# Kernel tuning notes

Measured on AMD Instinct MI355X. Metric: run time of the kernel, lower is better.

The kernel has to match this reference:

```python
import jax, jax.numpy as jnp
import numpy as np

B = 8192          # batch size
D = 128           # embedding_dim
R = 1000          # relation_dict_len
MARGIN = 1.0


def setup_inputs() -> dict:
    key = jax.random.key(0)
    k1, k2, k3, k4 = jax.random.split(key, 4)
    return {
        "positive_batch": jax.random.normal(k1, (B, 3, D), dtype=jnp.float32),
        "negative_batch": jax.random.normal(k2, (B, 3, D), dtype=jnp.float32),
        "r_idx": jax.random.randint(k3, (B,), 0, R),
        "rel_emb": jax.random.normal(k4, (R, D * D), dtype=jnp.float32),
    }


def _score(batch, Wr):
    # batch: (B, 3, D) -> h, r, t each (B, D); Wr: (B, D, D)
    h, r, t = batch[:, 0], batch[:, 1], batch[:, 2]
    d = jnp.abs(h + r - t)                       # (B, D)
    # x^T Wr x quadratic form per example, fused in one einsum
    return jnp.einsum('bi,bij,bj->b', d, Wr, d)  # (B,)


def reference(positive_batch, negative_batch, r_idx, rel_emb):
    # Gather per-example relation matrix (Wr built from positive relation,
    # reused for the negative score, as in the original module).
    Wr = rel_emb[r_idx].reshape(-1, D, D)        # (B, D, D)
    pos = _score(positive_batch, Wr)
    neg = _score(negative_batch, Wr)
    return jnp.mean(jax.nn.relu(MARGIN + pos - neg))
```

## Files before the change

kernel.cpp:

```cpp
#include <hip/hip_runtime.h>

#define BATCH 8192
#define DIM 128
#define NREL 1000
#define MARGIN 1.0f

#define WS_PA 0
#define WS_PB 8192
#define WS_ORDER 16384
#define ORDER_CAP 11264

__global__ __launch_bounds__(1024) void sort_kernel(const int* __restrict__ r_idx,
                                                    int* __restrict__ order) {
  __shared__ int s_cnt[1024];
  __shared__ int s_cur[1024];
  __shared__ int s_wsum[16];
  const int tid = threadIdx.x, lane = tid & 63, wave = tid >> 6;
  s_cnt[tid] = 0;
  __syncthreads();
  int my[8];
#pragma unroll
  for (int k = 0; k < 8; ++k) {
    my[k] = r_idx[tid + k * 1024];
    atomicAdd(&s_cnt[my[k]], 1);
  }
  __syncthreads();
  const int c = (s_cnt[tid] + 3) & ~3;
  int v = c;
#pragma unroll
  for (int o = 1; o < 64; o <<= 1) {
    int u = __shfl_up(v, o, 64);
    if (lane >= o) v += u;
  }
  if (lane == 63) s_wsum[wave] = v;
  __syncthreads();
  int woff = 0;
  for (int w = 0; w < wave; ++w) woff += s_wsum[w];
  s_cur[tid] = woff + v - c;
  for (int i = tid; i < ORDER_CAP; i += 1024) order[i] = -1;
  __syncthreads();
#pragma unroll
  for (int k = 0; k < 8; ++k) {
    int p = atomicAdd(&s_cur[my[k]], 1);
    order[p] = tid + k * 1024;
  }
}

__device__ inline float2 dvec(const float* __restrict__ b, int c0) {
  float2 h = *(const float2*)(b + c0);
  float2 r = *(const float2*)(b + DIM + c0);
  float2 t = *(const float2*)(b + 2 * DIM + c0);
  return make_float2(fabsf(h.x + r.x - t.x), fabsf(h.y + r.y - t.y));
}

__global__ __launch_bounds__(256) void score_kernel(
    const float* __restrict__ pos_b, const float* __restrict__ neg_b,
    const int* __restrict__ r_idx, const float* __restrict__ rel_emb,
    const int* __restrict__ order, float* __restrict__ pA,
    float* __restrict__ pB) {
  __shared__ float s_d[4][DIM][8];
  const int tid = threadIdx.x, lane = tid & 63, wave = tid >> 6;
  const int pair = wave >> 1, half = wave & 1;
  const int g = blockIdx.x * 2 + pair;
  int4 es = *(const int4*)(order + g * 4);
  if (es.x < 0) return;
  const int c0 = lane * 2;
  const int r = r_idx[es.x];
  const bool v1 = es.y >= 0, v2 = es.z >= 0, v3 = es.w >= 0;
  const int e1 = v1 ? es.y : es.x, e2 = v2 ? es.z : es.x, e3 = v3 ? es.w : es.x;

  const float2 z = make_float2(0.f, 0.f);
  float2 dp0 = dvec(pos_b + (size_t)es.x * 3 * DIM, c0);
  float2 dn0 = dvec(neg_b + (size_t)es.x * 3 * DIM, c0);
  float2 dp1 = v1 ? dvec(pos_b + (size_t)e1 * 3 * DIM, c0) : z;
  float2 dn1 = v1 ? dvec(neg_b + (size_t)e1 * 3 * DIM, c0) : z;
  float2 dp2 = v2 ? dvec(pos_b + (size_t)e2 * 3 * DIM, c0) : z;
  float2 dn2 = v2 ? dvec(neg_b + (size_t)e2 * 3 * DIM, c0) : z;
  float2 dp3 = v3 ? dvec(pos_b + (size_t)e3 * 3 * DIM, c0) : z;
  float2 dn3 = v3 ? dvec(neg_b + (size_t)e3 * 3 * DIM, c0) : z;

  *(float4*)&s_d[wave][c0][0]     = make_float4(dp0.x, dp1.x, dp2.x, dp3.x);
  *(float4*)&s_d[wave][c0][4]     = make_float4(dn0.x, dn1.x, dn2.x, dn3.x);
  *(float4*)&s_d[wave][c0 + 1][0] = make_float4(dp0.y, dp1.y, dp2.y, dp3.y);
  *(float4*)&s_d[wave][c0 + 1][4] = make_float4(dn0.y, dn1.y, dn2.y, dn3.y);

  const int colb = (lane & 31) * 4;
  const int rsel = lane >> 5;
  const int rowbase = half * 64;
  const float* W = rel_emb + (size_t)r * (DIM * DIM) +
                   (size_t)(rowbase + rsel) * DIM + colb;

  float4 fz = make_float4(0.f, 0.f, 0.f, 0.f);
  float4 ap0 = fz, ap1 = fz, ap2 = fz, ap3 = fz;
  float4 an0 = fz, an1 = fz, an2 = fz, an3 = fz;
#pragma unroll 4
  for (int it = 0; it < 32; ++it) {
    float4 wv = *(const float4*)(W + (size_t)(it * 2) * DIM);
    const int row = rowbase + it * 2 + rsel;
    float4 ddp = *(const float4*)&s_d[wave][row][0];
    float4 ddn = *(const float4*)&s_d[wave][row][4];
    ap0.x = fmaf(ddp.x, wv.x, ap0.x); ap0.y = fmaf(ddp.x, wv.y, ap0.y);
    ap0.z = fmaf(ddp.x, wv.z, ap0.z); ap0.w = fmaf(ddp.x, wv.w, ap0.w);
    ap1.x = fmaf(ddp.y, wv.x, ap1.x); ap1.y = fmaf(ddp.y, wv.y, ap1.y);
    ap1.z = fmaf(ddp.y, wv.z, ap1.z); ap1.w = fmaf(ddp.y, wv.w, ap1.w);
    ap2.x = fmaf(ddp.z, wv.x, ap2.x); ap2.y = fmaf(ddp.z, wv.y, ap2.y);
    ap2.z = fmaf(ddp.z, wv.z, ap2.z); ap2.w = fmaf(ddp.z, wv.w, ap2.w);
    ap3.x = fmaf(ddp.w, wv.x, ap3.x); ap3.y = fmaf(ddp.w, wv.y, ap3.y);
    ap3.z = fmaf(ddp.w, wv.z, ap3.z); ap3.w = fmaf(ddp.w, wv.w, ap3.w);
    an0.x = fmaf(ddn.x, wv.x, an0.x); an0.y = fmaf(ddn.x, wv.y, an0.y);
    an0.z = fmaf(ddn.x, wv.z, an0.z); an0.w = fmaf(ddn.x, wv.w, an0.w);
    an1.x = fmaf(ddn.y, wv.x, an1.x); an1.y = fmaf(ddn.y, wv.y, an1.y);
    an1.z = fmaf(ddn.y, wv.z, an1.z); an1.w = fmaf(ddn.y, wv.w, an1.w);
    an2.x = fmaf(ddn.z, wv.x, an2.x); an2.y = fmaf(ddn.z, wv.y, an2.y);
    an2.z = fmaf(ddn.z, wv.z, an2.z); an2.w = fmaf(ddn.z, wv.w, an2.w);
    an3.x = fmaf(ddn.w, wv.x, an3.x); an3.y = fmaf(ddn.w, wv.y, an3.y);
    an3.z = fmaf(ddn.w, wv.z, an3.z); an3.w = fmaf(ddn.w, wv.w, an3.w);
  }

  float s0 = 0.f, s1 = 0.f, s2 = 0.f, s3 = 0.f;
#define EPI(K, COMP)                                          \
  {                                                           \
    float4 dp4 = *(const float4*)&s_d[wave][colb + K][0];     \
    float4 dn4 = *(const float4*)&s_d[wave][colb + K][4];     \
    s0 += ap0.COMP * dp4.x - an0.COMP * dn4.x;                \
    s1 += ap1.COMP * dp4.y - an1.COMP * dn4.y;                \
    s2 += ap2.COMP * dp4.z - an2.COMP * dn4.z;                \
    s3 += ap3.COMP * dp4.w - an3.COMP * dn4.w;                \
  }
  EPI(0, x) EPI(1, y) EPI(2, z) EPI(3, w)
#undef EPI

#pragma unroll
  for (int o = 32; o > 0; o >>= 1) {
    s0 += __shfl_xor(s0, o, 64);
    s1 += __shfl_xor(s1, o, 64);
    s2 += __shfl_xor(s2, o, 64);
    s3 += __shfl_xor(s3, o, 64);
  }
  float* P = half ? pB : pA;
  if (lane == 0) {
    P[es.x] = s0;
    if (v1) P[es.y] = s1;
    if (v2) P[es.z] = s2;
    if (v3) P[es.w] = s3;
  }
}

__global__ __launch_bounds__(256) void reduce_kernel(const float* __restrict__ pA,
                                                     const float* __restrict__ pB,
                                                     float* __restrict__ out) {
  float acc = 0.f;
  for (int i = threadIdx.x; i < BATCH; i += 256) {
    float v = MARGIN + pA[i] + pB[i];
    acc += (v > 0.f) ? v : 0.f;
  }
#pragma unroll
  for (int o = 32; o > 0; o >>= 1) acc += __shfl_xor(acc, o, 64);
  __shared__ float s[4];
  const int lane = threadIdx.x & 63, wave = threadIdx.x >> 6;
  if (lane == 0) s[wave] = acc;
  __syncthreads();
  if (threadIdx.x == 0) out[0] = (s[0] + s[1] + s[2] + s[3]) * (1.0f / BATCH);
}

extern "C" void kernel_launch(void* const* d_in, const int* in_sizes, int n_in,
                              void* d_out, int out_size, void* d_ws, size_t ws_size,
                              hipStream_t stream) {
  const float* pos_b = (const float*)d_in[0];
  const float* neg_b = (const float*)d_in[1];
  const int* r_idx = (const int*)d_in[2];
  const float* rel_emb = (const float*)d_in[3];
  float* out = (float*)d_out;

  float* pA = (float*)d_ws + WS_PA;
  float* pB = (float*)d_ws + WS_PB;
  int* order = (int*)d_ws + WS_ORDER;

  sort_kernel<<<1, 1024, 0, stream>>>(r_idx, order);
  score_kernel<<<1400, 256, 0, stream>>>(pos_b, neg_b, r_idx, rel_emb, order,
                                         pA, pB);
  reduce_kernel<<<1, 256, 0, stream>>>(pA, pB, out);
}
```

Measured before the change: 46.45 us.

## Fuse final reduction into score kernel via last-block counter and remap blocks

Removes the separate reduce kernel launch by having the last score block, detected through an atomic counter reset in the sort kernel, perform the final ReLU-mean reduction. It also permutes the block-to-work mapping so consecutive physical blocks are spread across the sorted relation groups, presumably to balance load across XCDs. This adds an atomic plus fences per block and a serialized tail reduction on one block, in exchange for saving a launch gap.

```diff
diff --git a/kernel.cpp b/kernel.cpp
--- a/kernel.cpp
+++ b/kernel.cpp
@@ -4,18 +4,22 @@
 #define DIM 128
 #define NREL 1000
 #define MARGIN 1.0f
+#define GRID 1400
 
 #define WS_PA 0
 #define WS_PB 8192
 #define WS_ORDER 16384
+#define WS_CTR 27648
 #define ORDER_CAP 11264
 
 __global__ __launch_bounds__(1024) void sort_kernel(const int* __restrict__ r_idx,
-                                                    int* __restrict__ order) {
+                                                    int* __restrict__ order,
+                                                    int* __restrict__ ctr) {
   __shared__ int s_cnt[1024];
   __shared__ int s_cur[1024];
   __shared__ int s_wsum[16];
   const int tid = threadIdx.x, lane = tid & 63, wave = tid >> 6;
+  if (tid == 0) ctr[0] = 0;
   s_cnt[tid] = 0;
   __syncthreads();
   int my[8];
@@ -57,110 +61,121 @@
     const float* __restrict__ pos_b, const float* __restrict__ neg_b,
     const int* __restrict__ r_idx, const float* __restrict__ rel_emb,
     const int* __restrict__ order, float* __restrict__ pA,
-    float* __restrict__ pB) {
+    float* __restrict__ pB, int* __restrict__ ctr, float* __restrict__ out) {
   __shared__ float s_d[4][DIM][8];
+  __shared__ int s_last;
   const int tid = threadIdx.x, lane = tid & 63, wave = tid >> 6;
+  const int phys = blockIdx.x;
+  const int lb = (phys & 7) * (GRID / 8) + (phys >> 3);
   const int pair = wave >> 1, half = wave & 1;
-  const int g = blockIdx.x * 2 + pair;
+  const int g = lb * 2 + pair;
   int4 es = *(const int4*)(order + g * 4);
-  if (es.x < 0) return;
-  const int c0 = lane * 2;
-  const int r = r_idx[es.x];
-  const bool v1 = es.y >= 0, v2 = es.z >= 0, v3 = es.w >= 0;
-  const int e1 = v1 ? es.y : es.x, e2 = v2 ? es.z : es.x, e3 = v3 ? es.w : es.x;
 
-  const float2 z = make_float2(0.f, 0.f);
-  float2 dp0 = dvec(pos_b + (size_t)es.x * 3 * DIM, c0);
-  float2 dn0 = dvec(neg_b + (size_t)es.x * 3 * DIM, c0);
-  float2 dp1 = v1 ? dvec(pos_b + (size_t)e1 * 3 * DIM, c0) : z;
-  float2 dn1 = v1 ? dvec(neg_b + (size_t)e1 * 3 * DIM, c0) : z;
-  float2 dp2 = v2 ? dvec(pos_b + (size_t)e2 * 3 * DIM, c0) : z;
-  float2 dn2 = v2 ? dvec(neg_b + (size_t)e2 * 3 * DIM, c0) : z;
-  float2 dp3 = v3 ? dvec(pos_b + (size_t)e3 * 3 * DIM, c0) : z;
-  float2 dn3 = v3 ? dvec(neg_b + (size_t)e3 * 3 * DIM, c0) : z;
+  if (es.x >= 0) {
+    const int c0 = lane * 2;
+    const int r = r_idx[es.x];
+    const bool v1 = es.y >= 0, v2 = es.z >= 0, v3 = es.w >= 0;
+    const int e1 = v1 ? es.y : es.x, e2 = v2 ? es.z : es.x,
+              e3 = v3 ? es.w : es.x;
 
-  *(float4*)&s_d[wave][c0][0]     = make_float4(dp0.x, dp1.x, dp2.x, dp3.x);
-  *(float4*)&s_d[wave][c0][4]     = make_float4(dn0.x, dn1.x, dn2.x, dn3.x);
-  *(float4*)&s_d[wave][c0 + 1][0] = make_float4(dp0.y, dp1.y, dp2.y, dp3.y);
-  *(float4*)&s_d[wave][c0 + 1][4] = make_float4(dn0.y, dn1.y, dn2.y, dn3.y);
+    const float2 z = make_float2(0.f, 0.f);
+    float2 dp0 = dvec(pos_b + (size_t)es.x * 3 * DIM, c0);
+    float2 dn0 = dvec(neg_b + (size_t)es.x * 3 * DIM, c0);
+    float2 dp1 = v1 ? dvec(pos_b + (size_t)e1 * 3 * DIM, c0) : z;
+    float2 dn1 = v1 ? dvec(neg_b + (size_t)e1 * 3 * DIM, c0) : z;
+    float2 dp2 = v2 ? dvec(pos_b + (size_t)e2 * 3 * DIM, c0) : z;
+    float2 dn2 = v2 ? dvec(neg_b + (size_t)e2 * 3 * DIM, c0) : z;
+    float2 dp3 = v3 ? dvec(pos_b + (size_t)e3 * 3 * DIM, c0) : z;
+    float2 dn3 = v3 ? dvec(neg_b + (size_t)e3 * 3 * DIM, c0) : z;
 
-  const int colb = (lane & 31) * 4;
-  const int rsel = lane >> 5;
-  const int rowbase = half * 64;
-  const float* W = rel_emb + (size_t)r * (DIM * DIM) +
-                   (size_t)(rowbase + rsel) * DIM + colb;
+    *(float4*)&s_d[wave][c0][0]     = make_float4(dp0.x, dp1.x, dp2.x, dp3.x);
+    *(float4*)&s_d[wave][c0][4]     = make_float4(dn0.x, dn1.x, dn2.x, dn3.x);
+    *(float4*)&s_d[wave][c0 + 1][0] = make_float4(dp0.y, dp1.y, dp2.y, dp3.y);
+    *(float4*)&s_d[wave][c0 + 1][4] = make_float4(dn0.y, dn1.y, dn2.y, dn3.y);
 
-  float4 fz = make_float4(0.f, 0.f, 0.f, 0.f);
-  float4 ap0 = fz, ap1 = fz, ap2 = fz, ap3 = fz;
-  float4 an0 = fz, an1 = fz, an2 = fz, an3 = fz;
+    const int colb = (lane & 31) * 4;
+    const int rsel = lane >> 5;
+    const int rowbase = half * 64;
+    const float* W = rel_emb + (size_t)r * (DIM * DIM) +
+                     (size_t)(rowbase + rsel) * DIM + colb;
+
+    float4 fz = make_float4(0.f, 0.f, 0.f, 0.f);
+    float4 ap0 = fz, ap1 = fz, ap2 = fz, ap3 = fz;
+    float4 an0 = fz, an1 = fz, an2 = fz, an3 = fz;
 #pragma unroll 4
-  for (int it = 0; it < 32; ++it) {
-    float4 wv = *(const float4*)(W + (size_t)(it * 2) * DIM);
-    const int row = rowbase + it * 2 + rsel;
-    float4 ddp = *(const float4*)&s_d[wave][row][0];
-    float4 ddn = *(const float4*)&s_d[wave][row][4];
-    ap0.x = fmaf(ddp.x, wv.x, ap0.x); ap0.y = fmaf(ddp.x, wv.y, ap0.y);
-    ap0.z = fmaf(ddp.x, wv.z, ap0.z); ap0.w = fmaf(ddp.x, wv.w, ap0.w);
-    ap1.x = fmaf(ddp.y, wv.x, ap1.x); ap1.y = fmaf(ddp.y, wv.y, ap1.y);
-    ap1.z = fmaf(ddp.y, wv.z, ap1.z); ap1.w = fmaf(ddp.y, wv.w, ap1.w);
-    ap2.x = fmaf(ddp.z, wv.x, ap2.x); ap2.y = fmaf(ddp.z, wv.y, ap2.y);
-    ap2.z = fmaf(ddp.z, wv.z, ap2.z); ap2.w = fmaf(ddp.z, wv.w, ap2.w);
-    ap3.x = fmaf(ddp.w, wv.x, ap3.x); ap3.y = fmaf(ddp.w, wv.y, ap3.y);
-    ap3.z = fmaf(ddp.w, wv.z, ap3.z); ap3.w = fmaf(ddp.w, wv.w, ap3.w);
-    an0.x = fmaf(ddn.x, wv.x, an0.x); an0.y = fmaf(ddn.x, wv.y, an0.y);
-    an0.z = fmaf(ddn.x, wv.z, an0.z); an0.w = fmaf(ddn.x, wv.w, an0.w);
-    an1.x = fmaf(ddn.y, wv.x, an1.x); an1.y = fmaf(ddn.y, wv.y, an1.y);
-    an1.z = fmaf(ddn.y, wv.z, an1.z); an1.w = fmaf(ddn.y, wv.w, an1.w);
-    an2.x = fmaf(ddn.z, wv.x, an2.x); an2.y = fmaf(ddn.z, wv.y, an2.y);
-    an2.z = fmaf(ddn.z, wv.z, an2.z); an2.w = fmaf(ddn.z, wv.w, an2.w);
-    an3.x = fmaf(ddn.w, wv.x, an3.x); an3.y = fmaf(ddn.w, wv.y, an3.y);
-    an3.z = fmaf(ddn.w, wv.z, an3.z); an3.w = fmaf(ddn.w, wv.w, an3.w);
-  }
+    for (int it = 0; it < 32; ++it) {
+      float4 wv = *(const float4*)(W + (size_t)(it * 2) * DIM);
+      const int row = rowbase + it * 2 + rsel;
+      float4 ddp = *(const float4*)&s_d[wave][row][0];
+      float4 ddn = *(const float4*)&s_d[wave][row][4];
+      ap0.x = fmaf(ddp.x, wv.x, ap0.x); ap0.y = fmaf(ddp.x, wv.y, ap0.y);
+      ap0.z = fmaf(ddp.x, wv.z, ap0.z); ap0.w = fmaf(ddp.x, wv.w, ap0.w);
+      ap1.x = fmaf(ddp.y, wv.x, ap1.x); ap1.y = fmaf(ddp.y, wv.y, ap1.y);
+      ap1.z = fmaf(ddp.y, wv.z, ap1.z); ap1.w = fmaf(ddp.y, wv.w, ap1.w);
+      ap2.x = fmaf(ddp.z, wv.x, ap2.x); ap2.y = fmaf(ddp.z, wv.y, ap2.y);
+      ap2.z = fmaf(ddp.z, wv.z, ap2.z); ap2.w = fmaf(ddp.z, wv.w, ap2.w);
+      ap3.x = fmaf(ddp.w, wv.x, ap3.x); ap3.y = fmaf(ddp.w, wv.y, ap3.y);
+      ap3.z = fmaf(ddp.w, wv.z, ap3.z); ap3.w = fmaf(ddp.w, wv.w, ap3.w);
+      an0.x = fmaf(ddn.x, wv.x, an0.x); an0.y = fmaf(ddn.x, wv.y, an0.y);
+      an0.z = fmaf(ddn.x, wv.z, an0.z); an0.w = fmaf(ddn.x, wv.w, an0.w);
+      an1.x = fmaf(ddn.y, wv.x, an1.x); an1.y = fmaf(ddn.y, wv.y, an1.y);
+      an1.z = fmaf(ddn.y, wv.z, an1.z); an1.w = fmaf(ddn.y, wv.w, an1.w);
+      an2.x = fmaf(ddn.z, wv.x, an2.x); an2.y = fmaf(ddn.z, wv.y, an2.y);
+      an2.z = fmaf(ddn.z, wv.z, an2.z); an2.w = fmaf(ddn.z, wv.w, an2.w);
+      an3.x = fmaf(ddn.w, wv.x, an3.x); an3.y = fmaf(ddn.w, wv.y, an3.y);
+      an3.z = fmaf(ddn.w, wv.z, an3.z); an3.w = fmaf(ddn.w, wv.w, an3.w);
+    }
 
-  float s0 = 0.f, s1 = 0.f, s2 = 0.f, s3 = 0.f;
+    float s0 = 0.f, s1 = 0.f, s2 = 0.f, s3 = 0.f;
 #define EPI(K, COMP)                                          \
-  {                                                           \
-    float4 dp4 = *(const float4*)&s_d[wave][colb + K][0];     \
-    float4 dn4 = *(const float4*)&s_d[wave][colb + K][4];     \
-    s0 += ap0.COMP * dp4.x - an0.COMP * dn4.x;                \
-    s1 += ap1.COMP * dp4.y - an1.COMP * dn4.y;                \
-    s2 += ap2.COMP * dp4.z - an2.COMP * dn4.z;                \
-    s3 += ap3.COMP * dp4.w - an3.COMP * dn4.w;                \
-  }
-  EPI(0, x) EPI(1, y) EPI(2, z) EPI(3, w)
+    {                                                         \
+      float4 dp4 = *(const float4*)&s_d[wave][colb + K][0];   \
+      float4 dn4 = *(const float4*)&s_d[wave][colb + K][4];   \
+      s0 += ap0.COMP * dp4.x - an0.COMP * dn4.x;              \
+      s1 += ap1.COMP * dp4.y - an1.COMP * dn4.y;              \
+      s2 += ap2.COMP * dp4.z - an2.COMP * dn4.z;              \
+      s3 += ap3.COMP * dp4.w - an3.COMP * dn4.w;              \
+    }
+    EPI(0, x) EPI(1, y) EPI(2, z) EPI(3, w)
 #undef EPI
 
 #pragma unroll
-  for (int o = 32; o > 0; o >>= 1) {
-    s0 += __shfl_xor(s0, o, 64);
-    s1 += __shfl_xor(s1, o, 64);
-    s2 += __shfl_xor(s2, o, 64);
-    s3 += __shfl_xor(s3, o, 64);
+    for (int o = 32; o > 0; o >>= 1) {
+      s0 += __shfl_xor(s0, o, 64);
+      s1 += __shfl_xor(s1, o, 64);
+      s2 += __shfl_xor(s2, o, 64);
+      s3 += __shfl_xor(s3, o, 64);
+    }
+    float* P = half ? pB : pA;
+    if (lane == 0) {
+      P[es.x] = s0;
+      if (v1) P[es.y] = s1;
+      if (v2) P[es.z] = s2;
+      if (v3) P[es.w] = s3;
+    }
   }
-  float* P = half ? pB : pA;
-  if (lane == 0) {
-    P[es.x] = s0;
-    if (v1) P[es.y] = s1;
-    if (v2) P[es.z] = s2;
-    if (v3) P[es.w] = s3;
+
+  __syncthreads();
+  if (tid == 0) {
+    __threadfence();
+    s_last = (atomicAdd(ctr, 1) == GRID - 1);
   }
-}
-
-__global__ __launch_bounds__(256) void reduce_kernel(const float* __restrict__ pA,
-                                                     const float* __restrict__ pB,
-                                                     float* __restrict__ out) {
-  float acc = 0.f;
-  for (int i = threadIdx.x; i < BATCH; i += 256) {
-    float v = MARGIN + pA[i] + pB[i];
-    acc += (v > 0.f) ? v : 0.f;
+  __syncthreads();
+  if (s_last) {
+    __threadfence();
+    float acc = 0.f;
+    for (int i = tid; i < BATCH; i += 256) {
+      float v = MARGIN + pA[i] + pB[i];
+      acc += (v > 0.f) ? v : 0.f;
+    }
+#pragma unroll
+    for (int o = 32; o > 0; o >>= 1) acc += __shfl_xor(acc, o, 64);
+    if (lane == 0) s_d[0][0][wave] = acc;
+    __syncthreads();
+    if (tid == 0)
+      out[0] = (s_d[0][0][0] + s_d[0][0][1] + s_d[0][0][2] + s_d[0][0][3]) *
+               (1.0f / BATCH);
   }
-#pragma unroll
-  for (int o = 32; o > 0; o >>= 1) acc += __shfl_xor(acc, o, 64);
-  __shared__ float s[4];
-  const int lane = threadIdx.x & 63, wave = threadIdx.x >> 6;
-  if (lane == 0) s[wave] = acc;
-  __syncthreads();
-  if (threadIdx.x == 0) out[0] = (s[0] + s[1] + s[2] + s[3]) * (1.0f / BATCH);
 }
 
 extern "C" void kernel_launch(void* const* d_in, const int* in_sizes, int n_in,
@@ -175,9 +190,9 @@
   float* pA = (float*)d_ws + WS_PA;
   float* pB = (float*)d_ws + WS_PB;
   int* order = (int*)d_ws + WS_ORDER;
+  int* ctr = (int*)d_ws + WS_CTR;
 
-  sort_kernel<<<1, 1024, 0, stream>>>(r_idx, order);
-  score_kernel<<<1400, 256, 0, stream>>>(pos_b, neg_b, r_idx, rel_emb, order,
-                                         pA, pB);
-  reduce_kernel<<<1, 256, 0, stream>>>(pA, pB, out);
+  sort_kernel<<<1, 1024, 0, stream>>>(r_idx, order, ctr);
+  score_kernel<<<GRID, 256, 0, stream>>>(pos_b, neg_b, r_idx, rel_emb, order,
+                                         pA, pB, ctr, out);
 }
```

New measurement: 85.73 us. 84.6% more time.

## Process eight same-relation examples per block with four waves splitting W rows

Applied to the files above, without the earlier changes.

Examples are now padded into groups of eight sharing a relation instead of four, so each block loads its relation matrix once for eight examples, with the four waves each covering a quarter of the rows. Per-wave partial scores are combined in shared memory and written as one value per example, which removes the second partial array and shrinks the reduction. Blocks are remapped with a stride so neighbouring blocks spread across the grid. This raises register pressure from doubled accumulators and adds more padding lanes for relations with few examples.

```diff
diff --git a/kernel.cpp b/kernel.cpp
--- a/kernel.cpp
+++ b/kernel.cpp
@@ -4,11 +4,11 @@
 #define DIM 128
 #define NREL 1000
 #define MARGIN 1.0f
-
-#define WS_PA 0
-#define WS_PB 8192
-#define WS_ORDER 16384
-#define ORDER_CAP 11264
+#define GRID 1904
+#define ORDER_CAP 15232
+
+#define WS_PARTIAL 0
+#define WS_ORDER 8192
 
 __global__ __launch_bounds__(1024) void sort_kernel(const int* __restrict__ r_idx,
                                                     int* __restrict__ order) {
@@ -25,7 +25,7 @@
     atomicAdd(&s_cnt[my[k]], 1);
   }
   __syncthreads();
-  const int c = (s_cnt[tid] + 3) & ~3;
+  const int c = (s_cnt[tid] + 7) & ~7;
   int v = c;
 #pragma unroll
   for (int o = 1; o < 64; o <<= 1) {
@@ -56,76 +56,89 @@
 __global__ __launch_bounds__(256) void score_kernel(
     const float* __restrict__ pos_b, const float* __restrict__ neg_b,
     const int* __restrict__ r_idx, const float* __restrict__ rel_emb,
-    const int* __restrict__ order, float* __restrict__ pA,
-    float* __restrict__ pB) {
-  __shared__ float s_d[4][DIM][8];
+    const int* __restrict__ order, float* __restrict__ partial) {
+  __shared__ float s_d[DIM][16];
+  __shared__ float s_ps[4][8];
+  __shared__ int s_es[8];
   const int tid = threadIdx.x, lane = tid & 63, wave = tid >> 6;
-  const int pair = wave >> 1, half = wave & 1;
-  const int g = blockIdx.x * 2 + pair;
-  int4 es = *(const int4*)(order + g * 4);
-  if (es.x < 0) return;
+  const int phys = blockIdx.x;
+  const int g = (phys & 7) * (GRID / 8) + (phys >> 3);
+
+  if (order[g * 8] < 0) return;
+  if (tid < 8) s_es[tid] = order[g * 8 + tid];
+  __syncthreads();
+
   const int c0 = lane * 2;
-  const int r = r_idx[es.x];
-  const bool v1 = es.y >= 0, v2 = es.z >= 0, v3 = es.w >= 0;
-  const int e1 = v1 ? es.y : es.x, e2 = v2 ? es.z : es.x, e3 = v3 ? es.w : es.x;
-
-  const float2 z = make_float2(0.f, 0.f);
-  float2 dp0 = dvec(pos_b + (size_t)es.x * 3 * DIM, c0);
-  float2 dn0 = dvec(neg_b + (size_t)es.x * 3 * DIM, c0);
-  float2 dp1 = v1 ? dvec(pos_b + (size_t)e1 * 3 * DIM, c0) : z;
-  float2 dn1 = v1 ? dvec(neg_b + (size_t)e1 * 3 * DIM, c0) : z;
-  float2 dp2 = v2 ? dvec(pos_b + (size_t)e2 * 3 * DIM, c0) : z;
-  float2 dn2 = v2 ? dvec(neg_b + (size_t)e2 * 3 * DIM, c0) : z;
-  float2 dp3 = v3 ? dvec(pos_b + (size_t)e3 * 3 * DIM, c0) : z;
-  float2 dn3 = v3 ? dvec(neg_b + (size_t)e3 * 3 * DIM, c0) : z;
-
-  *(float4*)&s_d[wave][c0][0]     = make_float4(dp0.x, dp1.x, dp2.x, dp3.x);
-  *(float4*)&s_d[wave][c0][4]     = make_float4(dn0.x, dn1.x, dn2.x, dn3.x);
-  *(float4*)&s_d[wave][c0 + 1][0] = make_float4(dp0.y, dp1.y, dp2.y, dp3.y);
-  *(float4*)&s_d[wave][c0 + 1][4] = make_float4(dn0.y, dn1.y, dn2.y, dn3.y);
-
+  {
+    const int a = s_es[2 * wave], b = s_es[2 * wave + 1];
+    const bool va = a >= 0, vb = b >= 0;
+    const int ia = va ? a : s_es[0], ib = vb ? b : s_es[0];
+    const float2 z = make_float2(0.f, 0.f);
+    float2 dpa = va ? dvec(pos_b + (size_t)ia * 3 * DIM, c0) : z;
+    float2 dna = va ? dvec(neg_b + (size_t)ia * 3 * DIM, c0) : z;
+    float2 dpb = vb ? dvec(pos_b + (size_t)ib * 3 * DIM, c0) : z;
+    float2 dnb = vb ? dvec(neg_b + (size_t)ib * 3 * DIM, c0) : z;
+    *(float2*)&s_d[c0][2 * wave]         = make_float2(dpa.x, dpb.x);
+    *(float2*)&s_d[c0 + 1][2 * wave]     = make_float2(dpa.y, dpb.y);
+    *(float2*)&s_d[c0][8 + 2 * wave]     = make_float2(dna.x, dnb.x);
+    *(float2*)&s_d[c0 + 1][8 + 2 * wave] = make_float2(dna.y, dnb.y);
+  }
+  __syncthreads();
+
+  const int r = r_idx[s_es[0]];
   const int colb = (lane & 31) * 4;
   const int rsel = lane >> 5;
-  const int rowbase = half * 64;
+  const int rowbase = wave * 32;
   const float* W = rel_emb + (size_t)r * (DIM * DIM) +
                    (size_t)(rowbase + rsel) * DIM + colb;
 
-  float4 fz = make_float4(0.f, 0.f, 0.f, 0.f);
+  const float4 fz = make_float4(0.f, 0.f, 0.f, 0.f);
   float4 ap0 = fz, ap1 = fz, ap2 = fz, ap3 = fz;
+  float4 ap4 = fz, ap5 = fz, ap6 = fz, ap7 = fz;
   float4 an0 = fz, an1 = fz, an2 = fz, an3 = fz;
+  float4 an4 = fz, an5 = fz, an6 = fz, an7 = fz;
+
+#define FMA4(ACC, D, WV)                    \
+  ACC.x = fmaf(D, WV.x, ACC.x);             \
+  ACC.y = fmaf(D, WV.y, ACC.y);             \
+  ACC.z = fmaf(D, WV.z, ACC.z);             \
+  ACC.w = fmaf(D, WV.w, ACC.w);
+
 #pragma unroll 4
-  for (int it = 0; it < 32; ++it) {
+  for (int it = 0; it < 16; ++it) {
     float4 wv = *(const float4*)(W + (size_t)(it * 2) * DIM);
     const int row = rowbase + it * 2 + rsel;
-    float4 ddp = *(const float4*)&s_d[wave][row][0];
-    float4 ddn = *(const float4*)&s_d[wave][row][4];
-    ap0.x = fmaf(ddp.x, wv.x, ap0.x); ap0.y = fmaf(ddp.x, wv.y, ap0.y);
-    ap0.z = fmaf(ddp.x, wv.z, ap0.z); ap0.w = fmaf(ddp.x, wv.w, ap0.w);
-    ap1.x = fmaf(ddp.y, wv.x, ap1.x); ap1.y = fmaf(ddp.y, wv.y, ap1.y);
-    ap1.z = fmaf(ddp.y, wv.z, ap1.z); ap1.w = fmaf(ddp.y, wv.w, ap1.w);
-    ap2.x = fmaf(ddp.z, wv.x, ap2.x); ap2.y = fmaf(ddp.z, wv.y, ap2.y);
-    ap2.z = fmaf(ddp.z, wv.z, ap2.z); ap2.w = fmaf(ddp.z, wv.w, ap2.w);
-    ap3.x = fmaf(ddp.w, wv.x, ap3.x); ap3.y = fmaf(ddp.w, wv.y, ap3.y);
-    ap3.z = fmaf(ddp.w, wv.z, ap3.z); ap3.w = fmaf(ddp.w, wv.w, ap3.w);
-    an0.x = fmaf(ddn.x, wv.x, an0.x); an0.y = fmaf(ddn.x, wv.y, an0.y);
-    an0.z = fmaf(ddn.x, wv.z, an0.z); an0.w = fmaf(ddn.x, wv.w, an0.w);
-    an1.x = fmaf(ddn.y, wv.x, an1.x); an1.y = fmaf(ddn.y, wv.y, an1.y);
-    an1.z = fmaf(ddn.y, wv.z, an1.z); an1.w = fmaf(ddn.y, wv.w, an1.w);
-    an2.x = fmaf(ddn.z, wv.x, an2.x); an2.y = fmaf(ddn.z, wv.y, an2.y);
-    an2.z = fmaf(ddn.z, wv.z, an2.z); an2.w = fmaf(ddn.z, wv.w, an2.w);
-    an3.x = fmaf(ddn.w, wv.x, an3.x); an3.y = fmaf(ddn.w, wv.y, an3.y);
-    an3.z = fmaf(ddn.w, wv.z, an3.z); an3.w = fmaf(ddn.w, wv.w, an3.w);
-  }
+    float4 ddp0 = *(const float4*)&s_d[row][0];
+    float4 ddp1 = *(const float4*)&s_d[row][4];
+    float4 ddn0 = *(const float4*)&s_d[row][8];
+    float4 ddn1 = *(const float4*)&s_d[row][12];
+    FMA4(ap0, ddp0.x, wv) FMA4(ap1, ddp0.y, wv)
+    FMA4(ap2, ddp0.z, wv) FMA4(ap3, ddp0.w, wv)
+    FMA4(ap4, ddp1.x, wv) FMA4(ap5, ddp1.y, wv)
+    FMA4(ap6, ddp1.z, wv) FMA4(ap7, ddp1.w, wv)
+    FMA4(an0, ddn0.x, wv) FMA4(an1, ddn0.y, wv)
+    FMA4(an2, ddn0.z, wv) FMA4(an3, ddn0.w, wv)
+    FMA4(an4, ddn1.x, wv) FMA4(an5, ddn1.y, wv)
+    FMA4(an6, ddn1.z, wv) FMA4(an7, ddn1.w, wv)
+  }
+#undef FMA4
 
   float s0 = 0.f, s1 = 0.f, s2 = 0.f, s3 = 0.f;
-#define EPI(K, COMP)                                          \
-  {                                                           \
-    float4 dp4 = *(const float4*)&s_d[wave][colb + K][0];     \
-    float4 dn4 = *(const float4*)&s_d[wave][colb + K][4];     \
-    s0 += ap0.COMP * dp4.x - an0.COMP * dn4.x;                \
-    s1 += ap1.COMP * dp4.y - an1.COMP * dn4.y;                \
-    s2 += ap2.COMP * dp4.z - an2.COMP * dn4.z;                \
-    s3 += ap3.COMP * dp4.w - an3.COMP * dn4.w;                \
+  float s4 = 0.f, s5 = 0.f, s6 = 0.f, s7 = 0.f;
+#define EPI(K, COMP)                                         \
+  {                                                          \
+    float4 dp0 = *(const float4*)&s_d[colb + K][0];          \
+    float4 dp1 = *(const float4*)&s_d[colb + K][4];          \
+    float4 dn0 = *(const float4*)&s_d[colb + K][8];          \
+    float4 dn1 = *(const float4*)&s_d[colb + K][12];         \
+    s0 += ap0.COMP * dp0.x - an0.COMP * dn0.x;               \
+    s1 += ap1.COMP * dp0.y - an1.COMP * dn0.y;               \
+    s2 += ap2.COMP * dp0.z - an2.COMP * dn0.z;               \
+    s3 += ap3.COMP * dp0.w - an3.COMP * dn0.w;               \
+    s4 += ap4.COMP * dp1.x - an4.COMP * dn1.x;               \
+    s5 += ap5.COMP * dp1.y - an5.COMP * dn1.y;               \
+    s6 += ap6.COMP * dp1.z - an6.COMP * dn1.z;               \
+    s7 += ap7.COMP * dp1.w - an7.COMP * dn1.w;               \
   }
   EPI(0, x) EPI(1, y) EPI(2, z) EPI(3, w)
 #undef EPI
@@ -136,22 +149,30 @@
     s1 += __shfl_xor(s1, o, 64);
     s2 += __shfl_xor(s2, o, 64);
     s3 += __shfl_xor(s3, o, 64);
-  }
-  float* P = half ? pB : pA;
+    s4 += __shfl_xor(s4, o, 64);
+    s5 += __shfl_xor(s5, o, 64);
+    s6 += __shfl_xor(s6, o, 64);
+    s7 += __shfl_xor(s7, o, 64);
+  }
   if (lane == 0) {
-    P[es.x] = s0;
-    if (v1) P[es.y] = s1;
-    if (v2) P[es.z] = s2;
-    if (v3) P[es.w] = s3;
-  }
-}
-
-__global__ __launch_bounds__(256) void reduce_kernel(const float* __restrict__ pA,
-                                                     const float* __restrict__ pB,
+    s_ps[wave][0] = s0; s_ps[wave][1] = s1;
+    s_ps[wave][2] = s2; s_ps[wave][3] = s3;
+    s_ps[wave][4] = s4; s_ps[wave][5] = s5;
+    s_ps[wave][6] = s6; s_ps[wave][7] = s7;
+  }
+  __syncthreads();
+  if (tid < 8) {
+    const int e = s_es[tid];
+    if (e >= 0)
+      partial[e] = s_ps[0][tid] + s_ps[1][tid] + s_ps[2][tid] + s_ps[3][tid];
+  }
+}
+
+__global__ __launch_bounds__(256) void reduce_kernel(const float* __restrict__ partial,
                                                      float* __restrict__ out) {
   float acc = 0.f;
   for (int i = threadIdx.x; i < BATCH; i += 256) {
-    float v = MARGIN + pA[i] + pB[i];
+    float v = MARGIN + partial[i];
     acc += (v > 0.f) ? v : 0.f;
   }
 #pragma unroll
@@ -172,12 +193,11 @@
   const float* rel_emb = (const float*)d_in[3];
   float* out = (float*)d_out;
 
-  float* pA = (float*)d_ws + WS_PA;
-  float* pB = (float*)d_ws + WS_PB;
+  float* partial = (float*)d_ws + WS_PARTIAL;
   int* order = (int*)d_ws + WS_ORDER;
 
   sort_kernel<<<1, 1024, 0, stream>>>(r_idx, order);
-  score_kernel<<<1400, 256, 0, stream>>>(pos_b, neg_b, r_idx, rel_emb, order,
-                                         pA, pB);
-  reduce_kernel<<<1, 256, 0, stream>>>(pA, pB, out);
-}
+  score_kernel<<<GRID, 256, 0, stream>>>(pos_b, neg_b, r_idx, rel_emb, order,
+                                         partial);
+  reduce_kernel<<<1, 256, 0, stream>>>(partial, out);
+}
```

New measurement: 57.52 us. 23.8% more time.

## Pad shared d-vector layout, swizzle block order across XCDs, shuffle-based epilogue

Applied to the files above, without the earlier changes.

Stores each lane's d-values in shared memory at a 20-float stride to reduce bank conflicts, and gathers the epilogue's column d-values with wave shuffles instead of extra LDS reads. Remaps blockIdx so that consecutive logical blocks, which share relation matrices after sorting, land on the same XCD for better L2 reuse. Also raises the inner-loop unroll from 4 to 8. The remap assumes GRID is divisible by 8, and the higher unroll may raise register pressure.

```diff
diff --git a/kernel.cpp b/kernel.cpp
--- a/kernel.cpp
+++ b/kernel.cpp
@@ -4,11 +4,12 @@
 #define DIM 128
 #define NREL 1000
 #define MARGIN 1.0f
+#define GRID 1400
+#define ORDER_CAP 11264
 
 #define WS_PA 0
 #define WS_PB 8192
 #define WS_ORDER 16384
-#define ORDER_CAP 11264
 
 __global__ __launch_bounds__(1024) void sort_kernel(const int* __restrict__ r_idx,
                                                     int* __restrict__ order) {
@@ -58,12 +59,15 @@
     const int* __restrict__ r_idx, const float* __restrict__ rel_emb,
     const int* __restrict__ order, float* __restrict__ pA,
     float* __restrict__ pB) {
-  __shared__ float s_d[4][DIM][8];
+  __shared__ float s_d[4][64 * 20];
   const int tid = threadIdx.x, lane = tid & 63, wave = tid >> 6;
+  const int phys = blockIdx.x;
+  const int lb = (phys & 7) * (GRID / 8) + (phys >> 3);
   const int pair = wave >> 1, half = wave & 1;
-  const int g = blockIdx.x * 2 + pair;
+  const int g = lb * 2 + pair;
   int4 es = *(const int4*)(order + g * 4);
   if (es.x < 0) return;
+
   const int c0 = lane * 2;
   const int r = r_idx[es.x];
   const bool v1 = es.y >= 0, v2 = es.z >= 0, v3 = es.w >= 0;
@@ -79,56 +83,63 @@
   float2 dp3 = v3 ? dvec(pos_b + (size_t)e3 * 3 * DIM, c0) : z;
   float2 dn3 = v3 ? dvec(neg_b + (size_t)e3 * 3 * DIM, c0) : z;
 
-  *(float4*)&s_d[wave][c0][0]     = make_float4(dp0.x, dp1.x, dp2.x, dp3.x);
-  *(float4*)&s_d[wave][c0][4]     = make_float4(dn0.x, dn1.x, dn2.x, dn3.x);
-  *(float4*)&s_d[wave][c0 + 1][0] = make_float4(dp0.y, dp1.y, dp2.y, dp3.y);
-  *(float4*)&s_d[wave][c0 + 1][4] = make_float4(dn0.y, dn1.y, dn2.y, dn3.y);
+  {
+    float* myd = &s_d[wave][lane * 20];
+    *(float4*)(myd + 0)  = make_float4(dp0.x, dp1.x, dp2.x, dp3.x);
+    *(float4*)(myd + 4)  = make_float4(dn0.x, dn1.x, dn2.x, dn3.x);
+    *(float4*)(myd + 8)  = make_float4(dp0.y, dp1.y, dp2.y, dp3.y);
+    *(float4*)(myd + 12) = make_float4(dn0.y, dn1.y, dn2.y, dn3.y);
+  }
 
   const int colb = (lane & 31) * 4;
   const int rsel = lane >> 5;
-  const int rowbase = half * 64;
   const float* W = rel_emb + (size_t)r * (DIM * DIM) +
-                   (size_t)(rowbase + rsel) * DIM + colb;
+                   (size_t)(half * 64 + rsel) * DIM + colb;
+  const float* dptr = &s_d[wave][(half * 32) * 20 + rsel * 8];
 
-  float4 fz = make_float4(0.f, 0.f, 0.f, 0.f);
+  const float4 fz = make_float4(0.f, 0.f, 0.f, 0.f);
   float4 ap0 = fz, ap1 = fz, ap2 = fz, ap3 = fz;
   float4 an0 = fz, an1 = fz, an2 = fz, an3 = fz;
-#pragma unroll 4
+
+#define FMA4(ACC, D, WV)          \
+  ACC.x = fmaf(D, WV.x, ACC.x);   \
+  ACC.y = fmaf(D, WV.y, ACC.y);   \
+  ACC.z = fmaf(D, WV.z, ACC.z);   \
+  ACC.w = fmaf(D, WV.w, ACC.w);
+
+#pragma unroll 8
   for (int it = 0; it < 32; ++it) {
     float4 wv = *(const float4*)(W + (size_t)(it * 2) * DIM);
-    const int row = rowbase + it * 2 + rsel;
-    float4 ddp = *(const float4*)&s_d[wave][row][0];
-    float4 ddn = *(const float4*)&s_d[wave][row][4];
-    ap0.x = fmaf(ddp.x, wv.x, ap0.x); ap0.y = fmaf(ddp.x, wv.y, ap0.y);
-    ap0.z = fmaf(ddp.x, wv.z, ap0.z); ap0.w = fmaf(ddp.x, wv.w, ap0.w);
-    ap1.x = fmaf(ddp.y, wv.x, ap1.x); ap1.y = fmaf(ddp.y, wv.y, ap1.y);
-    ap1.z = fmaf(ddp.y, wv.z, ap1.z); ap1.w = fmaf(ddp.y, wv.w, ap1.w);
-    ap2.x = fmaf(ddp.z, wv.x, ap2.x); ap2.y = fmaf(ddp.z, wv.y, ap2.y);
-    ap2.z = fmaf(ddp.z, wv.z, ap2.z); ap2.w = fmaf(ddp.z, wv.w, ap2.w);
-    ap3.x = fmaf(ddp.w, wv.x, ap3.x); ap3.y = fmaf(ddp.w, wv.y, ap3.y);
-    ap3.z = fmaf(ddp.w, wv.z, ap3.z); ap3.w = fmaf(ddp.w, wv.w, ap3.w);
-    an0.x = fmaf(ddn.x, wv.x, an0.x); an0.y = fmaf(ddn.x, wv.y, an0.y);
-    an0.z = fmaf(ddn.x, wv.z, an0.z); an0.w = fmaf(ddn.x, wv.w, an0.w);
-    an1.x = fmaf(ddn.y, wv.x, an1.x); an1.y = fmaf(ddn.y, wv.y, an1.y);
-    an1.z = fmaf(ddn.y, wv.z, an1.z); an1.w = fmaf(ddn.y, wv.w, an1.w);
-    an2.x = fmaf(ddn.z, wv.x, an2.x); an2.y = fmaf(ddn.z, wv.y, an2.y);
-    an2.z = fmaf(ddn.z, wv.z, an2.z); an2.w = fmaf(ddn.z, wv.w, an2.w);
-    an3.x = fmaf(ddn.w, wv.x, an3.x); an3.y = fmaf(ddn.w, wv.y, an3.y);
-    an3.z = fmaf(ddn.w, wv.z, an3.z); an3.w = fmaf(ddn.w, wv.w, an3.w);
+    float4 ddp = *(const float4*)(dptr + it * 20);
+    float4 ddn = *(const float4*)(dptr + it * 20 + 4);
+    FMA4(ap0, ddp.x, wv) FMA4(ap1, ddp.y, wv)
+    FMA4(ap2, ddp.z, wv) FMA4(ap3, ddp.w, wv)
+    FMA4(an0, ddn.x, wv) FMA4(an1, ddn.y, wv)
+    FMA4(an2, ddn.z, wv) FMA4(an3, ddn.w, wv)
   }
+#undef FMA4
 
-  float s0 = 0.f, s1 = 0.f, s2 = 0.f, s3 = 0.f;
-#define EPI(K, COMP)                                          \
-  {                                                           \
-    float4 dp4 = *(const float4*)&s_d[wave][colb + K][0];     \
-    float4 dn4 = *(const float4*)&s_d[wave][colb + K][4];     \
-    s0 += ap0.COMP * dp4.x - an0.COMP * dn4.x;                \
-    s1 += ap1.COMP * dp4.y - an1.COMP * dn4.y;                \
-    s2 += ap2.COMP * dp4.z - an2.COMP * dn4.z;                \
-    s3 += ap3.COMP * dp4.w - an3.COMP * dn4.w;                \
-  }
-  EPI(0, x) EPI(1, y) EPI(2, z) EPI(3, w)
-#undef EPI
+  const int sl0 = (lane & 31) * 2, sl1 = sl0 + 1;
+#define GET4(OUT0, OUT1, OUT2, OUT3, V)   \
+  OUT0 = __shfl(V.x, sl0, 64);            \
+  OUT1 = __shfl(V.y, sl0, 64);            \
+  OUT2 = __shfl(V.x, sl1, 64);            \
+  OUT3 = __shfl(V.y, sl1, 64);
+  float a, b, c, d, e, f, gg, h;
+  float s0, s1, s2, s3;
+  GET4(a, b, c, d, dp0) GET4(e, f, gg, h, dn0)
+  s0 = ap0.x * a + ap0.y * b + ap0.z * c + ap0.w * d -
+       (an0.x * e + an0.y * f + an0.z * gg + an0.w * h);
+  GET4(a, b, c, d, dp1) GET4(e, f, gg, h, dn1)
+  s1 = ap1.x * a + ap1.y * b + ap1.z * c + ap1.w * d -
+       (an1.x * e + an1.y * f + an1.z * gg + an1.w * h);
+  GET4(a, b, c, d, dp2) GET4(e, f, gg, h, dn2)
+  s2 = ap2.x * a + ap2.y * b + ap2.z * c + ap2.w * d -
+       (an2.x * e + an2.y * f + an2.z * gg + an2.w * h);
+  GET4(a, b, c, d, dp3) GET4(e, f, gg, h, dn3)
+  s3 = ap3.x * a + ap3.y * b + ap3.z * c + ap3.w * d -
+       (an3.x * e + an3.y * f + an3.z * gg + an3.w * h);
+#undef GET4
 
 #pragma unroll
   for (int o = 32; o > 0; o >>= 1) {
@@ -177,7 +188,7 @@
   int* order = (int*)d_ws + WS_ORDER;
 
   sort_kernel<<<1, 1024, 0, stream>>>(r_idx, order);
-  score_kernel<<<1400, 256, 0, stream>>>(pos_b, neg_b, r_idx, rel_emb, order,
+  score_kernel<<<GRID, 256, 0, stream>>>(pos_b, neg_b, r_idx, rel_emb, order,
                                          pA, pB);
   reduce_kernel<<<1, 256, 0, stream>>>(pA, pB, out);
 }
```

New measurement: 43.97 us. 1.06x faster.
